# Optimization experiments

Hardware: AMD Instinct MI355X
Metric: run time of the kernel (lower is better)

The kernel has to match this reference:

```python
import jax, jax.numpy as jnp
import numpy as np

LR = 0.1
MOMENTUM = 0.95
NS_STEPS = 5


def _orthogonal(key, shape):
    # mimic nn.init.orthogonal_
    a = jax.random.normal(key, shape, jnp.float32)
    tall = shape[0] >= shape[1]
    q, r = jnp.linalg.qr(a if tall else a.T)
    q = q * jnp.sign(jnp.diagonal(r))
    return q if tall else q.T


def _ns5(G):
    # Newton-Schulz orthogonalization (Muon zeropower_via_newtonschulz5)
    a, b, c = 3.4445, -4.7750, 2.0315
    X = G / (jnp.linalg.norm(G) + 1e-7)
    transpose = G.shape[0] > G.shape[1]
    if transpose:
        X = X.T
    for _ in range(NS_STEPS):
        A = X @ X.T
        B = b * A + c * (A @ A)
        X = a * X + B @ X
    if transpose:
        X = X.T
    return X


def _muon_update(p, g, buf):
    buf = MOMENTUM * buf + g
    u = _ns5(g + MOMENTUM * buf)  # nesterov
    return p - LR * u, buf


def setup_inputs() -> dict:
    key = jax.random.key(0)
    k1, k2, k3, k4 = jax.random.split(key, 4)
    B, L, D_IN, D_H, D_OUT = 16, 4096, 512, 1024, 512
    return {
        "k": jax.random.normal(k1, (B, L, D_IN), jnp.float32),
        "v": jax.random.normal(k2, (B, L, D_OUT), jnp.float32),
        "w1": _orthogonal(k3, (D_IN, D_H)),
        "w2": _orthogonal(k4, (D_H, D_OUT)),
        "context_window": 8,
        "chunk_size": 64,
    }


def reference(k, v, w1, w2, context_window, chunk_size):
    B, L, D = k.shape
    n_chunks = L // chunk_size
    # [n_chunks, B, chunk, D] for scan over chunks
    kc = k[:, : n_chunks * chunk_size].reshape(B, n_chunks, chunk_size, D).transpose(1, 0, 2, 3)
    vc = v[:, : n_chunks * chunk_size].reshape(B, n_chunks, chunk_size, -1).transpose(1, 0, 2, 3)

    ones = jnp.ones((B, chunk_size), jnp.float32)
    mask = (jnp.tril(ones) - jnp.tril(ones, -context_window))[:, :, None]  # (B, chunk, 1)
    denom = B * chunk_size  # masked_diff2.numel()

    def chunk_loss(params, x, vt):
        w1_, w2_ = params
        l1 = jnp.tanh(x @ w1_)          # (B, chunk, d_h)
        out = l1 @ w2_                   # (B, chunk, d_out)
        diff2 = ((vt - out) ** 2).sum(-1, keepdims=True)
        return (diff2 * mask).sum() / denom, out

    def step(carry, inp):
        w1_, w2_, b1, b2 = carry
        x, vt = inp
        (_, out), (g1, g2) = jax.value_and_grad(chunk_loss, has_aux=True)((w1_, w2_), x, vt)
        w1n, b1 = _muon_update(w1_, g1, b1)
        w2n, b2 = _muon_update(w2_, g2, b2)
        return (w1n, w2n, b1, b2), out

    carry0 = (w1, w2, jnp.zeros_like(w1), jnp.zeros_like(w2))
    _, outs = jax.lax.scan(step, carry0, (kc, vc))
    return outs[-1]  # output of last chunk (pre-update weights of that chunk)
```

## Files before the change

kernel.cpp:

```cpp
#include <hip/hip_runtime.h>

#define D_ 512
#define H_ 1024
#define L_ 4096
#define CS_ 64
#define NCH_ 64
#define RACT_ 256
#define LR_ 0.1f
#define MOM_ 0.95f
#define NSA_ 3.4445f
#define NSB_ (-4.7750f)
#define NSC_ 2.0315f

#define MSZ_ ((size_t)D_ * H_)
#define ASZ_ ((size_t)D_ * D_)

using bf16x8 = __attribute__((ext_vector_type(8))) short;
using f32x4  = __attribute__((ext_vector_type(4))) float;
using s16x4  = __attribute__((ext_vector_type(4))) short;

__device__ __forceinline__ short f2bs(float f) {
  unsigned u = __builtin_bit_cast(unsigned, f);
  unsigned r = (u + 0x7fffu + ((u >> 16) & 1u)) >> 16;
  return (short)r;
}
__device__ __forceinline__ float bs2f(short s) {
  unsigned u = ((unsigned)(unsigned short)s) << 16;
  return __builtin_bit_cast(float, u);
}
__device__ __forceinline__ void split2(float v, short& h, short& l) {
  h = f2bs(v);
  l = f2bs(v - bs2f(h));
}

#define MFMA16(a, b, c) __builtin_amdgcn_mfma_f32_16x16x32_bf16(a, b, c, 0, 0, 0)

template <int K>
__device__ __forceinline__ f32x4 gemm_ks(
    const short* __restrict__ Ah, const short* __restrict__ Al, int lda,
    const short* __restrict__ Bh, const short* __restrict__ Bl, int ldb,
    int m0, int n0, float (*lds)[32][32], int& row, int& c0) {
  const int tid = threadIdx.x;
  const int w = tid >> 6, lane = tid & 63;
  const int lm = lane & 15, kq = lane >> 4;
  constexpr int KQ = K >> 2;
  f32x4 z = {0.f, 0.f, 0.f, 0.f};
  f32x4 acc[2][2] = {{z, z}, {z, z}};
  const size_t ao = (size_t)(m0 + lm) * lda + w * KQ + kq * 8;
  const size_t bo = (size_t)(n0 + lm) * ldb + w * KQ + kq * 8;
  const size_t ao1 = ao + (size_t)16 * lda;
  const size_t bo1 = bo + (size_t)16 * ldb;
#pragma unroll 4
  for (int k = 0; k < KQ; k += 32) {
    bf16x8 ah0 = *(const bf16x8*)(Ah + ao + k);
    bf16x8 ah1 = *(const bf16x8*)(Ah + ao1 + k);
    bf16x8 bh0 = *(const bf16x8*)(Bh + bo + k);
    bf16x8 bh1 = *(const bf16x8*)(Bh + bo1 + k);
    bf16x8 al0 = *(const bf16x8*)(Al + ao + k);
    bf16x8 al1 = *(const bf16x8*)(Al + ao1 + k);
    bf16x8 bl0 = *(const bf16x8*)(Bl + bo + k);
    bf16x8 bl1 = *(const bf16x8*)(Bl + bo1 + k);
    acc[0][0] = MFMA16(ah0, bh0, acc[0][0]);
    acc[0][1] = MFMA16(ah0, bh1, acc[0][1]);
    acc[1][0] = MFMA16(ah1, bh0, acc[1][0]);
    acc[1][1] = MFMA16(ah1, bh1, acc[1][1]);
    acc[0][0] = MFMA16(ah0, bl0, acc[0][0]);
    acc[0][1] = MFMA16(ah0, bl1, acc[0][1]);
    acc[1][0] = MFMA16(ah1, bl0, acc[1][0]);
    acc[1][1] = MFMA16(ah1, bl1, acc[1][1]);
    acc[0][0] = MFMA16(al0, bh0, acc[0][0]);
    acc[0][1] = MFMA16(al0, bh1, acc[0][1]);
    acc[1][0] = MFMA16(al1, bh0, acc[1][0]);
    acc[1][1] = MFMA16(al1, bh1, acc[1][1]);
  }
#pragma unroll
  for (int i = 0; i < 2; i++)
#pragma unroll
    for (int j = 0; j < 2; j++)
#pragma unroll
      for (int e = 0; e < 4; e++)
        lds[w][i * 16 + kq * 4 + e][j * 16 + lm] = acc[i][j][e];
  __syncthreads();
  row = tid >> 3;
  c0 = (tid & 7) * 4;
  f32x4 s = *(const f32x4*)&lds[0][row][c0];
  s += *(const f32x4*)&lds[1][row][c0];
  s += *(const f32x4*)&lds[2][row][c0];
  s += *(const f32x4*)&lds[3][row][c0];
  return s;
}

#define GEMM_SHARED __shared__ float lds[4][32][32];

struct P {
  const float *kin, *vin, *w1in, *w2in;
  float *w1f, *w2f, *buf1, *buf2t, *deriv, *partial;
  short *w1bth, *w1btl, *w2bh, *w2bl, *w2bth, *w2btl;
  short *Xph0, *Xpl0, *Xth0, *Xtl0, *Xph1, *Xpl1, *Xth1, *Xtl1;
  short *Ah, *Al, *Bmh, *Bml;
  short *l1h, *l1l, *l1Th, *l1Tl, *dOh, *dOl, *dOTh, *dOTl, *dpTh, *dpTl;
  short *xah, *xal, *xaTh, *xaTl;
  short *xfh, *xfl, *l1fh, *l1fl;
  float *out;
};

__device__ __forceinline__ void norm_scales(const float* __restrict__ partial,
                                            float* snorm, float* sred) {
  const int t = threadIdx.x;
#pragma unroll
  for (int jb = 0; jb < 2; jb++) {
    float v = partial[jb * 512 + t] + partial[jb * 512 + 256 + t];
    for (int off = 32; off > 0; off >>= 1) v += __shfl_down(v, off, 64);
    if ((t & 63) == 0) sred[t >> 6] = v;
    __syncthreads();
    if (t == 0)
      snorm[jb] = 1.f / (sqrtf(sred[0] + sred[1] + sred[2] + sred[3]) + 1e-7f);
    __syncthreads();
  }
}

__device__ __forceinline__ void kx_body(const P& p, int c) {
  for (int idx = blockIdx.x * blockDim.x + threadIdx.x; idx < RACT_ * D_;
       idx += gridDim.x * blockDim.x) {
    int r = idx >> 9, d = idx & 511;
    int b = r >> 4, t = r & 15;
    float v = p.kin[(size_t)(b * L_ + c * CS_ + t) * D_ + d];
    short h, l; split2(v, h, l);
    p.xah[idx] = h; p.xal[idx] = l;
    p.xaTh[(size_t)d * RACT_ + r] = h; p.xaTl[(size_t)d * RACT_ + r] = l;
  }
}

__device__ __forceinline__ void kxf_body(const P& p) {
  for (int idx = blockIdx.x * blockDim.x + threadIdx.x; idx < (int)MSZ_;
       idx += gridDim.x * blockDim.x) {
    int r = idx >> 9, d = idx & 511;
    int b = r >> 6, t = r & 63;
    float v = p.kin[(size_t)(b * L_ + (NCH_ - 1) * CS_ + t) * D_ + d];
    short h, l; split2(v, h, l);
    p.xfh[idx] = h; p.xfl[idx] = l;
  }
}

__global__ __launch_bounds__(256) void muon_init(P p) {
  int idx = blockIdx.x * 256 + threadIdx.x;
  float a = p.w1in[idx], b = p.w2in[idx];
  p.w1f[idx] = a; p.w2f[idx] = b;
  p.buf1[idx] = 0.f; p.buf2t[idx] = 0.f;
  short h, l;
  int d1 = idx >> 10, h1 = idx & 1023;
  split2(a, h, l);
  p.w1bth[(size_t)h1 * D_ + d1] = h; p.w1btl[(size_t)h1 * D_ + d1] = l;
  int h2 = idx >> 9, d2 = idx & 511;
  split2(b, h, l);
  p.w2bh[idx] = h; p.w2bl[idx] = l;
  p.w2bth[(size_t)d2 * H_ + h2] = h; p.w2btl[(size_t)d2 * H_ + h2] = l;
  if (idx < RACT_ * D_) {
    int r = idx >> 9, d = idx & 511;
    int b2 = r >> 4, t = r & 15;
    float v = p.kin[(size_t)(b2 * L_ + t) * D_ + d];
    split2(v, h, l);
    p.xah[idx] = h; p.xal[idx] = l;
    p.xaTh[(size_t)d * RACT_ + r] = h; p.xaTl[(size_t)d * RACT_ + r] = l;
  }
}

__global__ __launch_bounds__(256, 4) void muon_k1a(P p) {
  GEMM_SHARED
  const int m0 = (blockIdx.x >> 5) * 32, n0 = (blockIdx.x & 31) * 32;
  int row, c0;
  f32x4 s = gemm_ks<D_>(p.xah, p.xal, D_, p.w1bth, p.w1btl, D_,
                        m0, n0, lds, row, c0);
  int gm = m0 + row, gn0 = n0 + c0;
  s16x4 hv, lv; f32x4 dv;
#pragma unroll
  for (int cc = 0; cc < 4; cc++) {
    float l1v = tanhf(s[cc]);
    short h, l; split2(l1v, h, l);
    hv[cc] = h; lv[cc] = l; dv[cc] = 1.f - l1v * l1v;
    p.l1Th[(size_t)(gn0 + cc) * RACT_ + gm] = h;
    p.l1Tl[(size_t)(gn0 + cc) * RACT_ + gm] = l;
  }
  *(s16x4*)&p.l1h[(size_t)gm * H_ + gn0] = hv;
  *(s16x4*)&p.l1l[(size_t)gm * H_ + gn0] = lv;
  *(f32x4*)&p.deriv[(size_t)gm * H_ + gn0] = dv;
}

__global__ __launch_bounds__(256, 4) void muon_k1b(P p, int c) {
  GEMM_SHARED
  const int m0 = (blockIdx.x >> 4) * 32, n0 = (blockIdx.x & 15) * 32;
  int row, c0;
  f32x4 s = gemm_ks<H_>(p.l1h, p.l1l, H_, p.w2bth, p.w2btl, H_,
                        m0, n0, lds, row, c0);
  int gm = m0 + row, gn0 = n0 + c0;
  int b = gm >> 4, t = gm & 15;
  bool mk = (t <= b) && (b - t <= 7);
  f32x4 vt4 = {0.f, 0.f, 0.f, 0.f};
  if (mk) vt4 = *(const f32x4*)&p.vin[(size_t)(b * L_ + c * CS_ + t) * D_ + gn0];
  s16x4 hv, lv;
#pragma unroll
  for (int cc = 0; cc < 4; cc++) {
    float dv = mk ? (2.0f / 1024.0f) * (s[cc] - vt4[cc]) : 0.f;
    short h, l; split2(dv, h, l);
    hv[cc] = h; lv[cc] = l;
    p.dOTh[(size_t)(gn0 + cc) * RACT_ + gm] = h;
    p.dOTl[(size_t)(gn0 + cc) * RACT_ + gm] = l;
  }
  *(s16x4*)&p.dOh[(size_t)gm * D_ + gn0] = hv;
  *(s16x4*)&p.dOl[(size_t)gm * D_ + gn0] = lv;
}

__global__ __launch_bounds__(256, 4) void muon_k1c(P p) {
  GEMM_SHARED
  const int m0 = (blockIdx.x >> 5) * 32, n0 = (blockIdx.x & 31) * 32;
  int row, c0;
  f32x4 s = gemm_ks<D_>(p.dOh, p.dOl, D_, p.w2bh, p.w2bl, D_,
                        m0, n0, lds, row, c0);
  int gm = m0 + row, gn0 = n0 + c0;
  f32x4 dv = *(const f32x4*)&p.deriv[(size_t)gm * H_ + gn0];
#pragma unroll
  for (int cc = 0; cc < 4; cc++) {
    float dp = s[cc] * dv[cc];
    short h, l; split2(dp, h, l);
    p.dpTh[(size_t)(gn0 + cc) * RACT_ + gm] = h;
    p.dpTl[(size_t)(gn0 + cc) * RACT_ + gm] = l;
  }
}

__global__ __launch_bounds__(256, 4) void muon_k2(P p) {
  GEMM_SHARED
  __shared__ float sred[4];
  const int bid = blockIdx.x;
  const int job = bid >> 9, tt = bid & 511;
  const int m0 = (tt >> 5) * 32, n0 = (tt & 31) * 32;
  const short* Ah_ = job ? p.dOTh : p.xaTh;
  const short* Al_ = job ? p.dOTl : p.xaTl;
  const short* Bh_ = job ? p.l1Th : p.dpTh;
  const short* Bl_ = job ? p.l1Tl : p.dpTl;
  float* buf = job ? p.buf2t : p.buf1;
  short* xph = p.Xph0 + (size_t)job * MSZ_;
  short* xpl = p.Xpl0 + (size_t)job * MSZ_;
  short* xth = p.Xth0 + (size_t)job * MSZ_;
  short* xtl = p.Xtl0 + (size_t)job * MSZ_;
  int row, c0;
  f32x4 s = gemm_ks<RACT_>(Ah_, Al_, RACT_, Bh_, Bl_, RACT_, m0, n0, lds, row, c0);
  int gm = m0 + row, gn0 = n0 + c0;
  size_t idx0 = (size_t)gm * H_ + gn0;
  f32x4 bv = *(const f32x4*)&buf[idx0];
  s16x4 hv, lv;
  float part = 0.f;
#pragma unroll
  for (int cc = 0; cc < 4; cc++) {
    float bn = MOM_ * bv[cc] + s[cc];
    bv[cc] = bn;
    float g = s[cc] + MOM_ * bn;
    short h, l; split2(g, h, l);
    hv[cc] = h; lv[cc] = l;
    xth[(size_t)(gn0 + cc) * D_ + gm] = h;
    xtl[(size_t)(gn0 + cc) * D_ + gm] = l;
    part += g * g;
  }
  *(f32x4*)&buf[idx0] = bv;
  *(s16x4*)&xph[idx0] = hv;
  *(s16x4*)&xpl[idx0] = lv;
  for (int off = 32; off > 0; off >>= 1) part += __shfl_down(part, off, 64);
  if ((threadIdx.x & 63) == 0) sred[threadIdx.x >> 6] = part;
  __syncthreads();
  if (threadIdx.x == 0) p.partial[bid] = sred[0] + sred[1] + sred[2] + sred[3];
}

__global__ __launch_bounds__(256, 4) void muon_k4(P p, int cur, int it0) {
  GEMM_SHARED
  __shared__ float sred[4];
  __shared__ float snorm[2];
  if (it0) norm_scales(p.partial, snorm, sred);
  const int bid = blockIdx.x;
  const int job = bid >> 8, tt = bid & 255;
  const int m0 = (tt >> 4) * 32, n0 = (tt & 15) * 32;
  const short* Xph_ = cur ? p.Xph1 : p.Xph0;
  const short* Xpl_ = cur ? p.Xpl1 : p.Xpl0;
  const short* xh = Xph_ + (size_t)job * MSZ_;
  const short* xl = Xpl_ + (size_t)job * MSZ_;
  int row, c0;
  f32x4 s = gemm_ks<H_>(xh, xl, H_, xh, xl, H_, m0, n0, lds, row, c0);
  int gm = m0 + row, gn0 = n0 + c0;
  float sc = it0 ? (job ? snorm[1] * snorm[1] : snorm[0] * snorm[0]) : 1.f;
  short* ah = p.Ah + (size_t)job * ASZ_;
  short* al = p.Al + (size_t)job * ASZ_;
  s16x4 hv, lv;
#pragma unroll
  for (int cc = 0; cc < 4; cc++) {
    short h, l; split2(sc * s[cc], h, l);
    hv[cc] = h; lv[cc] = l;
  }
  *(s16x4*)&ah[(size_t)gm * D_ + gn0] = hv;
  *(s16x4*)&al[(size_t)gm * D_ + gn0] = lv;
}

__global__ __launch_bounds__(256, 4) void muon_k5(P p) {
  GEMM_SHARED
  const int bid = blockIdx.x;
  const int job = bid >> 8, tt = bid & 255;
  const int m0 = (tt >> 4) * 32, n0 = (tt & 15) * 32;
  const short* ah = p.Ah + (size_t)job * ASZ_;
  const short* al = p.Al + (size_t)job * ASZ_;
  int row, c0;
  f32x4 s = gemm_ks<D_>(ah, al, D_, ah, al, D_, m0, n0, lds, row, c0);
  int gm = m0 + row, gn0 = n0 + c0;
  s16x4 ahv = *(const s16x4*)&ah[(size_t)gm * D_ + gn0];
  s16x4 alv = *(const s16x4*)&al[(size_t)gm * D_ + gn0];
  short* bh = p.Bmh + (size_t)job * ASZ_;
  short* bl = p.Bml + (size_t)job * ASZ_;
  s16x4 hv, lv;
#pragma unroll
  for (int cc = 0; cc < 4; cc++) {
    float av = bs2f(ahv[cc]) + bs2f(alv[cc]);
    short h, l; split2(NSB_ * av + NSC_ * s[cc], h, l);
    hv[cc] = h; lv[cc] = l;
  }
  *(s16x4*)&bh[(size_t)gm * D_ + gn0] = hv;
  *(s16x4*)&bl[(size_t)gm * D_ + gn0] = lv;
}

__global__ __launch_bounds__(256, 4) void muon_k6(P p, int cur, int it0,
                                                  int last, int cnext) {
  GEMM_SHARED
  __shared__ float sred[4];
  __shared__ float snorm[2];
  if (it0) norm_scales(p.partial, snorm, sred);
  const int bid = blockIdx.x;
  const int job = bid >> 9, tt = bid & 511;
  const int m0 = (tt >> 5) * 32, n0 = (tt & 31) * 32;
  const short* Xph_ = cur ? p.Xph1 : p.Xph0;
  const short* Xpl_ = cur ? p.Xpl1 : p.Xpl0;
  const short* Xth_ = cur ? p.Xth1 : p.Xth0;
  const short* Xtl_ = cur ? p.Xtl1 : p.Xtl0;
  short* XphN = cur ? p.Xph0 : p.Xph1;
  short* XplN = cur ? p.Xpl0 : p.Xpl1;
  short* XthN = cur ? p.Xth0 : p.Xth1;
  short* XtlN = cur ? p.Xtl0 : p.Xtl1;
  const short* bmh = p.Bmh + (size_t)job * ASZ_;
  const short* bml = p.Bml + (size_t)job * ASZ_;
  int row, c0;
  f32x4 s = gemm_ks<D_>(bmh, bml, D_, Xth_ + job * MSZ_, Xtl_ + job * MSZ_,
                        D_, m0, n0, lds, row, c0);
  int gm = m0 + row, gn0 = n0 + c0;
  size_t idx0 = (size_t)gm * H_ + gn0;
  float scl = it0 ? (job ? snorm[1] : snorm[0]) : 1.f;
  s16x4 ph = *(const s16x4*)&Xph_[job * MSZ_ + idx0];
  s16x4 pl = *(const s16x4*)&Xpl_[job * MSZ_ + idx0];
  f32x4 xv;
#pragma unroll
  for (int cc = 0; cc < 4; cc++)
    xv[cc] = scl * (NSA_ * (bs2f(ph[cc]) + bs2f(pl[cc])) + s[cc]);
  if (!last) {
    s16x4 hv, lv;
#pragma unroll
    for (int cc = 0; cc < 4; cc++) {
      short h, l; split2(xv[cc], h, l);
      hv[cc] = h; lv[cc] = l;
      XthN[job * MSZ_ + (size_t)(gn0 + cc) * D_ + gm] = h;
      XtlN[job * MSZ_ + (size_t)(gn0 + cc) * D_ + gm] = l;
    }
    *(s16x4*)&XphN[job * MSZ_ + idx0] = hv;
    *(s16x4*)&XplN[job * MSZ_ + idx0] = lv;
  } else if (job == 0) {
    f32x4 wv = *(const f32x4*)&p.w1f[idx0];
#pragma unroll
    for (int cc = 0; cc < 4; cc++) {
      float nv = wv[cc] - LR_ * xv[cc];
      wv[cc] = nv;
      short h, l; split2(nv, h, l);
      p.w1bth[(size_t)(gn0 + cc) * D_ + gm] = h;
      p.w1btl[(size_t)(gn0 + cc) * D_ + gm] = l;
    }
    *(f32x4*)&p.w1f[idx0] = wv;
  } else {
    s16x4 hv, lv;
#pragma unroll
    for (int cc = 0; cc < 4; cc++) {
      size_t i2 = (size_t)(gn0 + cc) * D_ + gm;
      float nv = p.w2f[i2] - LR_ * xv[cc];
      p.w2f[i2] = nv;
      short h, l; split2(nv, h, l);
      p.w2bh[i2] = h; p.w2bl[i2] = l;
      hv[cc] = h; lv[cc] = l;
    }
    *(s16x4*)&p.w2bth[idx0] = hv;
    *(s16x4*)&p.w2btl[idx0] = lv;
  }
  if (last) {
    if (cnext < NCH_ - 1) kx_body(p, cnext);
    else kxf_body(p);
  }
}

__global__ __launch_bounds__(256, 4) void muon_k8a(P p) {
  GEMM_SHARED
  const int m0 = (blockIdx.x >> 5) * 32, n0 = (blockIdx.x & 31) * 32;
  int row, c0;
  f32x4 s = gemm_ks<D_>(p.xfh, p.xfl, D_, p.w1bth, p.w1btl, D_,
                        m0, n0, lds, row, c0);
  int gm = m0 + row, gn0 = n0 + c0;
  s16x4 hv, lv;
#pragma unroll
  for (int cc = 0; cc < 4; cc++) {
    short h, l; split2(tanhf(s[cc]), h, l);
    hv[cc] = h; lv[cc] = l;
  }
  *(s16x4*)&p.l1fh[(size_t)gm * H_ + gn0] = hv;
  *(s16x4*)&p.l1fl[(size_t)gm * H_ + gn0] = lv;
}

__global__ __launch_bounds__(256, 4) void muon_k8b(P p) {
  GEMM_SHARED
  const int m0 = (blockIdx.x >> 4) * 32, n0 = (blockIdx.x & 15) * 32;
  int row, c0;
  f32x4 s = gemm_ks<H_>(p.l1fh, p.l1fl, H_, p.w2bth, p.w2btl, H_,
                        m0, n0, lds, row, c0);
  int gm = m0 + row, gn0 = n0 + c0;
  *(f32x4*)&p.out[(size_t)gm * D_ + gn0] = s;
}

extern "C" void kernel_launch(void* const* d_in, const int* in_sizes, int n_in,
                              void* d_out, int out_size, void* d_ws, size_t ws_size,
                              hipStream_t stream) {
  char* pp = (char*)d_ws;
  auto take = [&](size_t bytes) {
    char* r = pp; pp += (bytes + 255) & ~(size_t)255; return r;
  };
  const size_t L1SZ = (size_t)RACT_ * H_;
  const size_t DOSZ = (size_t)RACT_ * D_;

  P p;
  p.kin  = (const float*)d_in[0];
  p.vin  = (const float*)d_in[1];
  p.w1in = (const float*)d_in[2];
  p.w2in = (const float*)d_in[3];
  p.out  = (float*)d_out;

  p.w1f   = (float*)take(MSZ_ * 4);
  p.w2f   = (float*)take(MSZ_ * 4);
  p.buf1  = (float*)take(MSZ_ * 4);
  p.buf2t = (float*)take(MSZ_ * 4);
  p.deriv = (float*)take(L1SZ * 4);
  p.partial = (float*)take(1024 * 4);
  p.w1bth = (short*)take(MSZ_ * 2);
  p.w1btl = (short*)take(MSZ_ * 2);
  p.w2bh  = (short*)take(MSZ_ * 2);
  p.w2bl  = (short*)take(MSZ_ * 2);
  p.w2bth = (short*)take(MSZ_ * 2);
  p.w2btl = (short*)take(MSZ_ * 2);
  p.Xph0 = (short*)take(2 * MSZ_ * 2);
  p.Xpl0 = (short*)take(2 * MSZ_ * 2);
  p.Xth0 = (short*)take(2 * MSZ_ * 2);
  p.Xtl0 = (short*)take(2 * MSZ_ * 2);
  p.Xph1 = (short*)take(2 * MSZ_ * 2);
  p.Xpl1 = (short*)take(2 * MSZ_ * 2);
  p.Xth1 = (short*)take(2 * MSZ_ * 2);
  p.Xtl1 = (short*)take(2 * MSZ_ * 2);
  p.Ah  = (short*)take(2 * ASZ_ * 2);
  p.Al  = (short*)take(2 * ASZ_ * 2);
  p.Bmh = (short*)take(2 * ASZ_ * 2);
  p.Bml = (short*)take(2 * ASZ_ * 2);
  p.l1h  = (short*)take(L1SZ * 2);
  p.l1l  = (short*)take(L1SZ * 2);
  p.l1Th = (short*)take(L1SZ * 2);
  p.l1Tl = (short*)take(L1SZ * 2);
  p.dOh  = (short*)take(DOSZ * 2);
  p.dOl  = (short*)take(DOSZ * 2);
  p.dOTh = (short*)take(DOSZ * 2);
  p.dOTl = (short*)take(DOSZ * 2);
  p.dpTh = (short*)take(L1SZ * 2);
  p.dpTl = (short*)take(L1SZ * 2);
  p.xah  = (short*)take(DOSZ * 2);
  p.xal  = (short*)take(DOSZ * 2);
  p.xaTh = (short*)take(DOSZ * 2);
  p.xaTl = (short*)take(DOSZ * 2);
  p.xfh  = p.Ah;
  p.xfl  = p.Al;
  p.l1fh = p.Xpl0;
  p.l1fl = p.Xph1;

  muon_init<<<2048, 256, 0, stream>>>(p);
  for (int c = 0; c < NCH_ - 1; c++) {
    muon_k1a<<<256, 256, 0, stream>>>(p);
    muon_k1b<<<128, 256, 0, stream>>>(p, c);
    muon_k1c<<<256, 256, 0, stream>>>(p);
    muon_k2<<<1024, 256, 0, stream>>>(p);
    for (int it = 0; it < 5; it++) {
      int cur = it & 1;
      muon_k4<<<512, 256, 0, stream>>>(p, cur, it == 0 ? 1 : 0);
      muon_k5<<<512, 256, 0, stream>>>(p);
      muon_k6<<<1024, 256, 0, stream>>>(p, cur, it == 0 ? 1 : 0,
                                        it == 4 ? 1 : 0, c + 1);
    }
  }
  muon_k8a<<<1024, 256, 0, stream>>>(p);
  muon_k8b<<<512, 256, 0, stream>>>(p);
}
```

Before: 17.00 ms.

## Coalesce transposed stores via LDS and exploit symmetry in Gram GEMMs

Transposed bf16 hi/lo outputs, which used to be written with strided scalar stores, are now staged through shared memory and written as coalesced 4-wide vectors. The A=XX^T and A@A kernels compute only upper-triangular tiles (136 per job instead of 256) and mirror off-diagonal tiles with a transposed store. The w2 fp32 master copy is kept in the transposed layout so its update is a vector access. The cost is extra syncthreads and LDS reuse per block, plus a small loop in each block to map its index to a triangular tile.

```diff
diff --git a/kernel.cpp b/kernel.cpp
--- a/kernel.cpp
+++ b/kernel.cpp
@@ -92,9 +92,30 @@
 
 #define GEMM_SHARED __shared__ float lds[4][32][32];
 
+__device__ __forceinline__ void store_T(
+    void* ldsraw, int row, int c0, const s16x4& hv, const s16x4& lv,
+    short* __restrict__ th, short* __restrict__ tl, int ldt, int m0, int n0) {
+  short (*sh)[36] = (short(*)[36])ldsraw;
+  short (*sl)[36] = (short(*)[36])ldsraw + 32;
+  __syncthreads();
+#pragma unroll
+  for (int cc = 0; cc < 4; cc++) {
+    sh[row][c0 + cc] = hv[cc];
+    sl[row][c0 + cc] = lv[cc];
+  }
+  __syncthreads();
+  const int tr = threadIdx.x >> 3;
+  const int tc = (threadIdx.x & 7) * 4;
+  s16x4 oh, ol;
+#pragma unroll
+  for (int j = 0; j < 4; j++) { oh[j] = sh[tc + j][tr]; ol[j] = sl[tc + j][tr]; }
+  *(s16x4*)&th[(size_t)(n0 + tr) * ldt + m0 + tc] = oh;
+  *(s16x4*)&tl[(size_t)(n0 + tr) * ldt + m0 + tc] = ol;
+}
+
 struct P {
   const float *kin, *vin, *w1in, *w2in;
-  float *w1f, *w2f, *buf1, *buf2t, *deriv, *partial;
+  float *w1f, *w2f , *buf1, *buf2t, *deriv, *partial;
   short *w1bth, *w1btl, *w2bh, *w2bl, *w2bth, *w2btl;
   short *Xph0, *Xpl0, *Xth0, *Xtl0, *Xph1, *Xpl1, *Xth1, *Xtl1;
   short *Ah, *Al, *Bmh, *Bml;
@@ -145,13 +166,14 @@
 __global__ __launch_bounds__(256) void muon_init(P p) {
   int idx = blockIdx.x * 256 + threadIdx.x;
   float a = p.w1in[idx], b = p.w2in[idx];
-  p.w1f[idx] = a; p.w2f[idx] = b;
+  p.w1f[idx] = a;
   p.buf1[idx] = 0.f; p.buf2t[idx] = 0.f;
   short h, l;
   int d1 = idx >> 10, h1 = idx & 1023;
   split2(a, h, l);
   p.w1bth[(size_t)h1 * D_ + d1] = h; p.w1btl[(size_t)h1 * D_ + d1] = l;
   int h2 = idx >> 9, d2 = idx & 511;
+  p.w2f[(size_t)d2 * H_ + h2] = b;
   split2(b, h, l);
   p.w2bh[idx] = h; p.w2bl[idx] = l;
   p.w2bth[(size_t)d2 * H_ + h2] = h; p.w2btl[(size_t)d2 * H_ + h2] = l;
@@ -178,12 +200,11 @@
     float l1v = tanhf(s[cc]);
     short h, l; split2(l1v, h, l);
     hv[cc] = h; lv[cc] = l; dv[cc] = 1.f - l1v * l1v;
-    p.l1Th[(size_t)(gn0 + cc) * RACT_ + gm] = h;
-    p.l1Tl[(size_t)(gn0 + cc) * RACT_ + gm] = l;
   }
   *(s16x4*)&p.l1h[(size_t)gm * H_ + gn0] = hv;
   *(s16x4*)&p.l1l[(size_t)gm * H_ + gn0] = lv;
   *(f32x4*)&p.deriv[(size_t)gm * H_ + gn0] = dv;
+  store_T(lds, row, c0, hv, lv, p.l1Th, p.l1Tl, RACT_, m0, n0);
 }
 
 __global__ __launch_bounds__(256, 4) void muon_k1b(P p, int c) {
@@ -203,11 +224,10 @@
     float dv = mk ? (2.0f / 1024.0f) * (s[cc] - vt4[cc]) : 0.f;
     short h, l; split2(dv, h, l);
     hv[cc] = h; lv[cc] = l;
-    p.dOTh[(size_t)(gn0 + cc) * RACT_ + gm] = h;
-    p.dOTl[(size_t)(gn0 + cc) * RACT_ + gm] = l;
   }
   *(s16x4*)&p.dOh[(size_t)gm * D_ + gn0] = hv;
   *(s16x4*)&p.dOl[(size_t)gm * D_ + gn0] = lv;
+  store_T(lds, row, c0, hv, lv, p.dOTh, p.dOTl, RACT_, m0, n0);
 }
 
 __global__ __launch_bounds__(256, 4) void muon_k1c(P p) {
@@ -218,13 +238,14 @@
                         m0, n0, lds, row, c0);
   int gm = m0 + row, gn0 = n0 + c0;
   f32x4 dv = *(const f32x4*)&p.deriv[(size_t)gm * H_ + gn0];
+  s16x4 hv, lv;
 #pragma unroll
   for (int cc = 0; cc < 4; cc++) {
     float dp = s[cc] * dv[cc];
     short h, l; split2(dp, h, l);
-    p.dpTh[(size_t)(gn0 + cc) * RACT_ + gm] = h;
-    p.dpTl[(size_t)(gn0 + cc) * RACT_ + gm] = l;
-  }
+    hv[cc] = h; lv[cc] = l;
+  }
+  store_T(lds, row, c0, hv, lv, p.dpTh, p.dpTl, RACT_, m0, n0);
 }
 
 __global__ __launch_bounds__(256, 4) void muon_k2(P p) {
@@ -240,8 +261,6 @@
   float* buf = job ? p.buf2t : p.buf1;
   short* xph = p.Xph0 + (size_t)job * MSZ_;
   short* xpl = p.Xpl0 + (size_t)job * MSZ_;
-  short* xth = p.Xth0 + (size_t)job * MSZ_;
-  short* xtl = p.Xtl0 + (size_t)job * MSZ_;
   int row, c0;
   f32x4 s = gemm_ks<RACT_>(Ah_, Al_, RACT_, Bh_, Bl_, RACT_, m0, n0, lds, row, c0);
   int gm = m0 + row, gn0 = n0 + c0;
@@ -256,13 +275,13 @@
     float g = s[cc] + MOM_ * bn;
     short h, l; split2(g, h, l);
     hv[cc] = h; lv[cc] = l;
-    xth[(size_t)(gn0 + cc) * D_ + gm] = h;
-    xtl[(size_t)(gn0 + cc) * D_ + gm] = l;
     part += g * g;
   }
   *(f32x4*)&buf[idx0] = bv;
   *(s16x4*)&xph[idx0] = hv;
   *(s16x4*)&xpl[idx0] = lv;
+  store_T(lds, row, c0, hv, lv, p.Xth0 + (size_t)job * MSZ_,
+          p.Xtl0 + (size_t)job * MSZ_, D_, m0, n0);
   for (int off = 32; off > 0; off >>= 1) part += __shfl_down(part, off, 64);
   if ((threadIdx.x & 63) == 0) sred[threadIdx.x >> 6] = part;
   __syncthreads();
@@ -275,8 +294,12 @@
   __shared__ float snorm[2];
   if (it0) norm_scales(p.partial, snorm, sred);
   const int bid = blockIdx.x;
-  const int job = bid >> 8, tt = bid & 255;
-  const int m0 = (tt >> 4) * 32, n0 = (tt & 15) * 32;
+  const int job = bid >= 136;
+  int tt = job ? bid - 136 : bid;
+  int mt = 0;
+  while (tt >= 16 - mt) { tt -= 16 - mt; mt++; }
+  const int nt = mt + tt;
+  const int m0 = mt * 32, n0 = nt * 32;
   const short* Xph_ = cur ? p.Xph1 : p.Xph0;
   const short* Xpl_ = cur ? p.Xpl1 : p.Xpl0;
   const short* xh = Xph_ + (size_t)job * MSZ_;
@@ -295,13 +318,18 @@
   }
   *(s16x4*)&ah[(size_t)gm * D_ + gn0] = hv;
   *(s16x4*)&al[(size_t)gm * D_ + gn0] = lv;
+  if (mt != nt) store_T(lds, row, c0, hv, lv, ah, al, D_, m0, n0);
 }
 
 __global__ __launch_bounds__(256, 4) void muon_k5(P p) {
   GEMM_SHARED
   const int bid = blockIdx.x;
-  const int job = bid >> 8, tt = bid & 255;
-  const int m0 = (tt >> 4) * 32, n0 = (tt & 15) * 32;
+  const int job = bid >= 136;
+  int tt = job ? bid - 136 : bid;
+  int mt = 0;
+  while (tt >= 16 - mt) { tt -= 16 - mt; mt++; }
+  const int nt = mt + tt;
+  const int m0 = mt * 32, n0 = nt * 32;
   const short* ah = p.Ah + (size_t)job * ASZ_;
   const short* al = p.Al + (size_t)job * ASZ_;
   int row, c0;
@@ -320,6 +348,7 @@
   }
   *(s16x4*)&bh[(size_t)gm * D_ + gn0] = hv;
   *(s16x4*)&bl[(size_t)gm * D_ + gn0] = lv;
+  if (mt != nt) store_T(lds, row, c0, hv, lv, bh, bl, D_, m0, n0);
 }
 
 __global__ __launch_bounds__(256, 4) void muon_k6(P p, int cur, int it0,
@@ -359,35 +388,37 @@
     for (int cc = 0; cc < 4; cc++) {
       short h, l; split2(xv[cc], h, l);
       hv[cc] = h; lv[cc] = l;
-      XthN[job * MSZ_ + (size_t)(gn0 + cc) * D_ + gm] = h;
-      XtlN[job * MSZ_ + (size_t)(gn0 + cc) * D_ + gm] = l;
     }
     *(s16x4*)&XphN[job * MSZ_ + idx0] = hv;
     *(s16x4*)&XplN[job * MSZ_ + idx0] = lv;
+    store_T(lds, row, c0, hv, lv, XthN + job * MSZ_, XtlN + job * MSZ_,
+            D_, m0, n0);
   } else if (job == 0) {
     f32x4 wv = *(const f32x4*)&p.w1f[idx0];
+    s16x4 hv, lv;
 #pragma unroll
     for (int cc = 0; cc < 4; cc++) {
       float nv = wv[cc] - LR_ * xv[cc];
       wv[cc] = nv;
       short h, l; split2(nv, h, l);
-      p.w1bth[(size_t)(gn0 + cc) * D_ + gm] = h;
-      p.w1btl[(size_t)(gn0 + cc) * D_ + gm] = l;
+      hv[cc] = h; lv[cc] = l;
     }
     *(f32x4*)&p.w1f[idx0] = wv;
+    store_T(lds, row, c0, hv, lv, p.w1bth, p.w1btl, D_, m0, n0);
   } else {
+    f32x4 wv = *(const f32x4*)&p.w2f[idx0];
     s16x4 hv, lv;
 #pragma unroll
     for (int cc = 0; cc < 4; cc++) {
-      size_t i2 = (size_t)(gn0 + cc) * D_ + gm;
-      float nv = p.w2f[i2] - LR_ * xv[cc];
-      p.w2f[i2] = nv;
+      float nv = wv[cc] - LR_ * xv[cc];
+      wv[cc] = nv;
       short h, l; split2(nv, h, l);
-      p.w2bh[i2] = h; p.w2bl[i2] = l;
       hv[cc] = h; lv[cc] = l;
     }
+    *(f32x4*)&p.w2f[idx0] = wv;
     *(s16x4*)&p.w2bth[idx0] = hv;
     *(s16x4*)&p.w2btl[idx0] = lv;
+    store_T(lds, row, c0, hv, lv, p.w2bh, p.w2bl, D_, m0, n0);
   }
   if (last) {
     if (cnext < NCH_ - 1) kx_body(p, cnext);
@@ -490,8 +521,8 @@
     muon_k2<<<1024, 256, 0, stream>>>(p);
     for (int it = 0; it < 5; it++) {
       int cur = it & 1;
-      muon_k4<<<512, 256, 0, stream>>>(p, cur, it == 0 ? 1 : 0);
-      muon_k5<<<512, 256, 0, stream>>>(p);
+      muon_k4<<<272, 256, 0, stream>>>(p, cur, it == 0 ? 1 : 0);
+      muon_k5<<<272, 256, 0, stream>>>(p);
       muon_k6<<<1024, 256, 0, stream>>>(p, cur, it == 0 ? 1 : 0,
                                         it == 4 ? 1 : 0, c + 1);
     }
```

Result: no change. 16.97 ms (-0.2%).
